# Performance work log

Hardware: AMD Instinct MI355X
Metric: run time of the kernel (lower is better)

Reference implementation:

```python
import jax, jax.numpy as jnp
import numpy as np

DPH, NH = 64, 4           # dim_per_head, num_head -> dim_total = 256
ALPHA_CONV = 0.1          # LeakyReLU alpha in DarknetConv2D_BN_Leaky
ALPHA_DENSE = 0.3         # Keras LeakyReLU default alpha (Dense activation)


def _leaky(x, a):
    return jnp.where(x > 0, x, a * x)


def _cbl(x, W, g, b):
    """1x1 conv (no bias) + inference BatchNorm (folded affine) + LeakyReLU(0.1)."""
    y = jnp.einsum('nwhc,cd->nwhd', x, W)
    return _leaky(y * g + b, ALPHA_CONV)


def setup_inputs() -> dict:
    key = jax.random.key(0)
    ks = jax.random.split(key, 26)
    N, Wg, Hg, C = 16, 64, 64, 256
    D = DPH * NH

    def n(k, shape, s=1.0):
        return jax.random.normal(k, shape, jnp.float32) * s

    return {
        'inputs': n(ks[0], (N, Wg, Hg, C)),
        'style':  n(ks[1], (N, C)),
        'W_dense': n(ks[2], (C, C), 0.05),
        'Wq_c': n(ks[3], (C, D), 0.05), 'gq_c': 1.0 + n(ks[4], (D,), 0.02), 'bq_c': n(ks[5], (D,), 0.02),
        'Wk_c': n(ks[6], (C, D), 0.05), 'gk_c': 1.0 + n(ks[7], (D,), 0.02), 'bk_c': n(ks[8], (D,), 0.02),
        'Wv_c': n(ks[9], (C, D), 0.05), 'gv_c': 1.0 + n(ks[10], (D,), 0.02), 'bv_c': n(ks[11], (D,), 0.02),
        'Wq_p': n(ks[12], (C, D), 0.05), 'gq_p': 1.0 + n(ks[13], (D,), 0.02), 'bq_p': n(ks[14], (D,), 0.02),
        'Wk_p': n(ks[15], (C, D), 0.05), 'gk_p': 1.0 + n(ks[16], (D,), 0.02), 'bk_p': n(ks[17], (D,), 0.02),
        'Wv_p': n(ks[18], (C, D), 0.05), 'gv_p': 1.0 + n(ks[19], (D,), 0.02), 'bv_p': n(ks[20], (D,), 0.02),
        'W_ch':  n(ks[21], (2 * D, D), 0.02),
        'W_pos': n(ks[22], (2 * D, NH), 0.02),
        'W_out': n(ks[23], (2 * D, C), 0.05),
        'g_out': 1.0 + n(ks[24], (C,), 0.02),
        'b_out': n(ks[25], (C,), 0.02),
    }


def reference(inputs, style, W_dense,
              Wq_c, gq_c, bq_c, Wk_c, gk_c, bk_c, Wv_c, gv_c, bv_c,
              Wq_p, gq_p, bq_p, Wk_p, gk_p, bk_p, Wv_p, gv_p, bv_p,
              W_ch, W_pos, W_out, g_out, b_out):
    N, Wg, Hg, C = inputs.shape
    D = DPH * NH
    scale = 1.0 / jnp.sqrt(jnp.float32(DPH))

    # style -> query feature, [N,1,1,C]
    q0 = _leaky(style @ W_dense, ALPHA_DENSE)[:, None, None, :]

    # ---------- channel-wise attention branch ----------
    qc = _cbl(q0, Wq_c, gq_c, bq_c)          # [N,1,1,D]
    kc = _cbl(inputs, Wk_c, gk_c, bk_c)      # [N,W,H,D]
    vc = _cbl(inputs, Wv_c, gv_c, bv_c)      # [N,W,H,D]
    catc = jnp.concatenate([jnp.broadcast_to(qc, kc.shape), kc], axis=-1)  # [N,W,H,2D]
    # einsum('awhd,awhdc->ac') with w broadcast over a,w,h == plain contraction
    a_c = jnp.einsum('nwhd,dc->nc', catc, W_ch) * scale                     # [N,D]
    a_c = jax.nn.softmax(a_c.reshape(N, DPH, NH), axis=1).reshape(N, 1, 1, D)
    o_ch = a_c * vc                                                          # [N,W,H,D]

    # ---------- position-wise attention branch ----------
    qp = _cbl(q0, Wq_p, gq_p, bq_p)
    kp = _cbl(inputs, Wk_p, gk_p, bk_p)
    vp = _cbl(inputs, Wv_p, gv_p, bv_p)
    catp = jnp.concatenate([jnp.broadcast_to(qp, kp.shape), kp], axis=-1)   # [N,W,H,2D]
    a_p = jnp.einsum('nwhd,dm->nwhm', catp, W_pos) * scale                  # [N,W,H,NH]
    a_p = jax.nn.softmax(a_p.reshape(N, Wg * Hg, NH), axis=1)
    a_p = a_p.reshape(N, Wg, Hg, NH, 1)
    o_pos = (a_p * vp.reshape(N, Wg, Hg, NH, DPH)).reshape(N, Wg, Hg, D)

    # ---------- fuse + output 1x1 conv ----------
    out = _cbl(jnp.concatenate([o_ch, o_pos], axis=-1), W_out, g_out, b_out)  # [N,W,H,C]
    return out
```

## Files before the change

### kernel.cpp

```cpp
#include <hip/hip_runtime.h>
#include <hip/hip_bf16.h>

#define PTOT  65536
#define SCALE 0.125f

typedef __attribute__((ext_vector_type(8))) short short8;
typedef __attribute__((ext_vector_type(4))) float f32x4;

__device__ __forceinline__ float leaky(float x, float a) { return x > 0.f ? x : a * x; }

__device__ __forceinline__ unsigned short f2bfbits(float f) {
    __hip_bfloat16 h = __float2bfloat16(f); unsigned short u;
    __builtin_memcpy(&u, &h, 2); return u;
}

__device__ __forceinline__ void gld16(const void* g, void* l) {
    __builtin_amdgcn_global_load_lds(
        (const __attribute__((address_space(1))) unsigned int*)g,
        (__attribute__((address_space(3))) unsigned int*)l, 16, 0, 0);
}

__device__ __forceinline__ void mfma_step64(const char* Aseg, const char* Bs,
                                            int l, int wm, int wn, f32x4 acc[2][4])
{
#pragma unroll
    for (int ks = 0; ks < 2; ++ks) {
        short8 af[2], bfr[4];
        const int c = ks * 4 + (l >> 4);
        const int sw = ((c ^ (l & 7)) << 4);
#pragma unroll
        for (int mf = 0; mf < 2; ++mf)
            af[mf] = *(const short8*)(Aseg + (wm * 32 + mf * 16 + (l & 15)) * 128 + sw);
#pragma unroll
        for (int nf = 0; nf < 4; ++nf)
            bfr[nf] = *(const short8*)(Bs + (wn * 64 + nf * 16 + (l & 15)) * 128 + sw);
#pragma unroll
        for (int mf = 0; mf < 2; ++mf)
#pragma unroll
            for (int nf = 0; nf < 4; ++nf)
                acc[mf][nf] = __builtin_amdgcn_mfma_f32_16x16x32_bf16(af[mf], bfr[nf], acc[mf][nf], 0, 0, 0);
    }
}

__device__ __forceinline__ void stageB(const __hip_bfloat16* Bt, int ldk, int k0,
                                       char* Bs, int w, int l, int cg)
{
#pragma unroll
    for (int pass = 0; pass < 4; ++pass) {
        const int col = w * 8 + (l >> 3) + pass * 64;
        gld16(Bt + (size_t)col * ldk + k0 + cg * 8, Bs + (w * 8 + pass * 64) * 128);
    }
}

__device__ __forceinline__ void stageA64(const __hip_bfloat16* Abf, int pix0, int k0,
                                         char* dst, int w, int l, int cg)
{
    const int row = w * 8 + (l >> 3);
    gld16(Abf + (size_t)(pix0 + row) * 256 + k0 + cg * 8, dst + w * 8 * 128);
}

template<int MODE>
__device__ __forceinline__ void k1_body(int bb, int t,
    const float* __restrict__ vin, const float* __restrict__ W,
    const float* __restrict__ g, const float* __restrict__ bv,
    float* __restrict__ vout, float* s0, float (*pr)[32])
{
    const int n = bb >> 3, c0 = (bb & 7) * 32;
    if (t < 256) s0[t] = vin[n * 256 + t];
    __syncthreads();
    const int kp = t >> 5, ci = t & 31, c = c0 + ci;
    float a = 0.f;
#pragma unroll 8
    for (int i = 0; i < 32; ++i) {
        const int k = kp * 32 + i;
        a += s0[k] * W[k * 256 + c];
    }
    pr[kp][ci] = a;
    __syncthreads();
    if (t < 32) {
        float s = 0.f;
#pragma unroll
        for (int q = 0; q < 8; ++q) s += pr[q][t];
        const int cc = c0 + t;
        if constexpr (MODE == 0)      vout[n * 256 + cc] = leaky(s, 0.3f);
        else if constexpr (MODE == 1) vout[n * 256 + cc] = leaky(s * g[cc] + bv[cc], 0.1f);
        else                          vout[n * 256 + cc] = 4096.f * s;
    }
}

template<int MODE>
__global__ __launch_bounds__(256) void k1g(
    const float* __restrict__ vin, const float* __restrict__ W,
    const float* __restrict__ g, const float* __restrict__ bv,
    float* __restrict__ vout)
{
    __shared__ float s0[256];
    __shared__ float pr[8][32];
    k1_body<MODE>(blockIdx.x, threadIdx.x, vin, W, g, bv, vout, s0, pr);
}

__global__ __launch_bounds__(256) void kW_cvt(
    const float* __restrict__ W0, const float* __restrict__ W1,
    const float* __restrict__ W2, const float* __restrict__ W3,
    const float* __restrict__ Wout,
    __hip_bfloat16* __restrict__ WT4, __hip_bfloat16* __restrict__ WoutT,
    const float* __restrict__ style, const float* __restrict__ W_dense,
    float* __restrict__ s1ws)
{
    __shared__ float s0[256];
    __shared__ float pr[8][32];
    const int b = blockIdx.x, t = threadIdx.x;
    if (b < 1024) {
        const int w = b >> 8, c = b & 255;
        const float* W = (w == 0) ? W0 : (w == 1) ? W1 : (w == 2) ? W2 : W3;
        WT4[((size_t)w * 256 + c) * 256 + t] = __float2bfloat16(W[t * 256 + c]);
    } else if (b < 1280) {
        const int c = b - 1024;
        WoutT[(size_t)c * 512 + t]       = __float2bfloat16(Wout[t * 256 + c]);
        WoutT[(size_t)c * 512 + t + 256] = __float2bfloat16(Wout[(t + 256) * 256 + c]);
    } else {
        k1_body<0>(b - 1280, t, style, W_dense, nullptr, nullptr, s1ws, s0, pr);
    }
}

__global__ __launch_bounds__(512, 4) void kA(
    const float* __restrict__ in, __hip_bfloat16* __restrict__ in_bf,
    const __hip_bfloat16* __restrict__ BkcT, const __hip_bfloat16* __restrict__ BkpT,
    const float* __restrict__ gkc, const float* __restrict__ bkc,
    const float* __restrict__ gkp, const float* __restrict__ bkp,
    const float* __restrict__ W_pos,
    float* __restrict__ partial, float* __restrict__ logits)
{
    __shared__ alignas(16) char smem[73728];
    char* Afull = smem;
    char* Bs    = smem + 32768;
    float* wpos_s = (float*)(smem + 65536);
    float* sc     = (float*)(smem + 69632);

    const int t = threadIdx.x, l = t & 63, w = t >> 6;
    const int pix0 = blockIdx.x * 64;

    for (int e = t; e < 1024; e += 512) wpos_s[e] = W_pos[1024 + e];

    {
        const int row = t >> 3, c = t & 7;
#pragma unroll
        for (int seg = 0; seg < 4; ++seg) {
            const float* p = in + (size_t)(pix0 + row) * 256 + seg * 64 + c * 8;
            const float4 x0 = *(const float4*)p, x1 = *(const float4*)(p + 4);
            short8 v;
            v[0]=(short)f2bfbits(x0.x); v[1]=(short)f2bfbits(x0.y); v[2]=(short)f2bfbits(x0.z); v[3]=(short)f2bfbits(x0.w);
            v[4]=(short)f2bfbits(x1.x); v[5]=(short)f2bfbits(x1.y); v[6]=(short)f2bfbits(x1.z); v[7]=(short)f2bfbits(x1.w);
            *(short8*)(Afull + seg * 8192 + row * 128 + ((c ^ (row & 7)) << 4)) = v;
            *(short8*)(in_bf + (size_t)(pix0 + row) * 256 + seg * 64 + c * 8) = v;
        }
    }

    f32x4 acc[4][4];
#pragma unroll
    for (int i = 0; i < 4; ++i)
#pragma unroll
        for (int j = 0; j < 4; ++j) acc[i][j] = (f32x4)0.f;

    for (int s = 0; s < 8; ++s) {
        __syncthreads();
        {
            const int cg = (l & 3) ^ ((l >> 3) & 3);
#pragma unroll
            for (int p = 0; p < 4; ++p) {
                const int col = w * 16 + (l >> 2) + p * 128;
                const __hip_bfloat16* src = (p < 2)
                    ? BkcT + (size_t)col * 256
                    : BkpT + (size_t)(col - 256) * 256;
                gld16(src + s * 32 + cg * 8, Bs + (size_t)(w * 16 + p * 128) * 64);
            }
        }
        __syncthreads();
        {
            const int c8 = (s & 1) * 4 + (l >> 4);
            const char* Aseg = Afull + (s >> 1) * 8192;
            short8 af[4], bfr[4];
#pragma unroll
            for (int mf = 0; mf < 4; ++mf) {
                const int row = mf * 16 + (l & 15);
                af[mf] = *(const short8*)(Aseg + row * 128 + ((c8 ^ (row & 7)) << 4));
            }
#pragma unroll
            for (int nf = 0; nf < 4; ++nf) {
                const int brow = w * 64 + nf * 16 + (l & 15);
                bfr[nf] = *(const short8*)(Bs + brow * 64 + (((l >> 4) ^ ((brow >> 1) & 3)) << 4));
            }
#pragma unroll
            for (int mf = 0; mf < 4; ++mf)
#pragma unroll
                for (int nf = 0; nf < 4; ++nf)
                    acc[mf][nf] = __builtin_amdgcn_mfma_f32_16x16x32_bf16(af[mf], bfr[nf], acc[mf][nf], 0, 0, 0);
        }
    }

    if (w < 4) {
#pragma unroll
        for (int nf = 0; nf < 4; ++nf) {
            const int col = w * 64 + nf * 16 + (l & 15);
            const float g = gkc[col], bb = bkc[col];
            float cs = 0.f;
#pragma unroll
            for (int mf = 0; mf < 4; ++mf)
#pragma unroll
                for (int r = 0; r < 4; ++r) cs += leaky(acc[mf][nf][r] * g + bb, 0.1f);
            cs += __shfl_xor(cs, 16);
            cs += __shfl_xor(cs, 32);
            if (l < 16) partial[(size_t)blockIdx.x * 256 + col] = cs;
        }
    } else {
#pragma unroll
        for (int mf = 0; mf < 4; ++mf)
#pragma unroll
            for (int r = 0; r < 4; ++r) {
                const int row = mf * 16 + (l >> 4) * 4 + r;
                float pm0 = 0.f, pm1 = 0.f, pm2 = 0.f, pm3 = 0.f;
#pragma unroll
                for (int nf = 0; nf < 4; ++nf) {
                    const int kcol = (w - 4) * 64 + nf * 16 + (l & 15);
                    const float g = gkp[kcol], bb = bkp[kcol];
                    const float v = leaky(acc[mf][nf][r] * g + bb, 0.1f);
                    pm0 += v * wpos_s[kcol * 4 + 0];
                    pm1 += v * wpos_s[kcol * 4 + 1];
                    pm2 += v * wpos_s[kcol * 4 + 2];
                    pm3 += v * wpos_s[kcol * 4 + 3];
                }
#pragma unroll
                for (int mask = 1; mask <= 8; mask <<= 1) {
                    pm0 += __shfl_xor(pm0, mask);
                    pm1 += __shfl_xor(pm1, mask);
                    pm2 += __shfl_xor(pm2, mask);
                    pm3 += __shfl_xor(pm3, mask);
                }
                if ((l & 15) == 0) {
                    float* sp = &sc[row * 16 + (w - 4)];
                    sp[0] = pm0; sp[4] = pm1; sp[8] = pm2; sp[12] = pm3;
                }
            }
    }
    __syncthreads();
    if (t < 256) {
        const int row = t >> 2, m = t & 3;
        const float sum = sc[row * 16 + m * 4 + 0] + sc[row * 16 + m * 4 + 1]
                        + sc[row * 16 + m * 4 + 2] + sc[row * 16 + m * 4 + 3];
        logits[(size_t)(pix0 + row) * 4 + m] = SCALE * sum;
    }
}

__global__ __launch_bounds__(256) void k2bc(
    const float* __restrict__ partial,
    const float* __restrict__ acq, const float* __restrict__ W_ch,
    float* __restrict__ a_c, float* __restrict__ lg)
{
    const int t = threadIdx.x;
    if (blockIdx.x < 16) {
        __shared__ float ks[256], lgs[256];
        const int n = blockIdx.x;
        float s = 0.f;
        for (int tt = 0; tt < 64; ++tt) s += partial[(size_t)(n * 64 + tt) * 256 + t];
        ks[t] = s;
        __syncthreads();
        float bot = 0.f;
        for (int d = 0; d < 256; ++d) bot += ks[d] * W_ch[(256 + d) * 256 + t];
        const float L = SCALE * (acq[n * 256 + t] + bot);
        lgs[t] = L;
        __syncthreads();
        const int nh = t & 3;
        float mx = -1e30f;
        for (int i = 0; i < 64; ++i) mx = fmaxf(mx, lgs[i * 4 + nh]);
        float sum = 0.f;
        for (int i = 0; i < 64; ++i) sum += __expf(lgs[i * 4 + nh] - mx);
        a_c[n * 256 + t] = __expf(L - mx) / sum;
    } else {
        __shared__ float r[256];
        const int bb = blockIdx.x - 16;
        const int n = bb >> 2, m = bb & 3;
        const int base = n * 4096;
        float v[16];
        float mx = -1e30f;
#pragma unroll
        for (int i = 0; i < 16; ++i) {
            v[i] = lg[(size_t)(base + i * 256 + t) * 4 + m];
            mx = fmaxf(mx, v[i]);
        }
        r[t] = mx; __syncthreads();
        for (int s = 128; s > 0; s >>= 1) { if (t < s) r[t] = fmaxf(r[t], r[t + s]); __syncthreads(); }
        mx = r[0]; __syncthreads();
        float sum = 0.f;
#pragma unroll
        for (int i = 0; i < 16; ++i) { v[i] = __expf(v[i] - mx); sum += v[i]; }
        r[t] = sum; __syncthreads();
        for (int s = 128; s > 0; s >>= 1) { if (t < s) r[t] += r[t + s]; __syncthreads(); }
        const float rinv = 1.f / r[0];
#pragma unroll
        for (int i = 0; i < 16; ++i) lg[(size_t)(base + i * 256 + t) * 4 + m] = v[i] * rinv;
    }
}

__global__ __launch_bounds__(512, 4) void kB(
    const __hip_bfloat16* __restrict__ Abf,
    const __hip_bfloat16* __restrict__ BvcT, const __hip_bfloat16* __restrict__ BvpT,
    const __hip_bfloat16* __restrict__ WoutT,
    const float* __restrict__ gvc, const float* __restrict__ bvc,
    const float* __restrict__ gvp, const float* __restrict__ bvp,
    const float* __restrict__ a_c, const float* __restrict__ apos,
    const float* __restrict__ g_out, const float* __restrict__ b_out,
    float* __restrict__ outp)
{
    __shared__ alignas(16) char smem[75776];
    char* As   = smem;
    char* Bs   = smem + 8192;
    char* A2   = smem + 40960;
    float* ac_s = (float*)(smem + 73728);
    float* ap_s = (float*)(smem + 74752);

    const int t = threadIdx.x, l = t & 63, w = t >> 6;
    const int wm = w >> 2, wn = w & 3;
    const int pix0 = blockIdx.x * 64;
    const int n = pix0 >> 12;
    const int cg = (l & 7) ^ ((l >> 3) & 7);

    if (t < 256) {
        ac_s[t] = a_c[n * 256 + t];
        ap_s[t] = apos[(size_t)pix0 * 4 + t];
    }

    f32x4 acc1c[2][4], acc1p[2][4], acc2[2][4];
#pragma unroll
    for (int i = 0; i < 2; ++i)
#pragma unroll
        for (int j = 0; j < 4; ++j) {
            acc1c[i][j] = (f32x4)0.f;
            acc1p[i][j] = (f32x4)0.f;
            acc2[i][j]  = (f32x4)0.f;
        }

    for (int s = 0; s < 4; ++s) {
        __syncthreads();
        stageA64(Abf, pix0, s * 64, As, w, l, cg);
        stageB(BvcT, 256, s * 64, Bs, w, l, cg);
        stageB(BvpT, 256, s * 64, A2, w, l, cg);
        __syncthreads();
        mfma_step64(As, Bs, l, wm, wn, acc1c);
        mfma_step64(As, A2, l, wm, wn, acc1p);
    }
    __syncthreads();

#pragma unroll
    for (int nf = 0; nf < 4; ++nf) {
        const int col = wn * 64 + nf * 16 + (l & 15);
        const float g = gvc[col], bb = bvc[col];
        const int c2 = (col & 63) >> 3, cb = (col & 7) * 2;
        const float sc_c = ac_s[col];
#pragma unroll
        for (int mf = 0; mf < 2; ++mf)
#pragma unroll
            for (int r = 0; r < 4; ++r) {
                const int row = wm * 32 + mf * 16 + (l >> 4) * 4 + r;
                float v = leaky(acc1c[mf][nf][r] * g + bb, 0.1f) * sc_c;
                *(unsigned short*)(A2 + wn * 8192 + row * 128
                                   + ((c2 ^ (row & 7)) << 4) + cb) = f2bfbits(v);
            }
    }
    for (int s = 0; s < 4; ++s) {
        __syncthreads();
        stageB(WoutT, 512, s * 64, Bs, w, l, cg);
        __syncthreads();
        mfma_step64(A2 + s * 8192, Bs, l, wm, wn, acc2);
    }
    __syncthreads();
#pragma unroll
    for (int nf = 0; nf < 4; ++nf) {
        const int col = wn * 64 + nf * 16 + (l & 15);
        const float g = gvp[col], bb = bvp[col];
        const int c2 = (col & 63) >> 3, cb = (col & 7) * 2;
#pragma unroll
        for (int mf = 0; mf < 2; ++mf)
#pragma unroll
            for (int r = 0; r < 4; ++r) {
                const int row = wm * 32 + mf * 16 + (l >> 4) * 4 + r;
                float v = leaky(acc1p[mf][nf][r] * g + bb, 0.1f) * ap_s[row * 4 + wn];
                *(unsigned short*)(A2 + wn * 8192 + row * 128
                                   + ((c2 ^ (row & 7)) << 4) + cb) = f2bfbits(v);
            }
    }
    for (int s = 0; s < 4; ++s) {
        __syncthreads();
        stageB(WoutT, 512, 256 + s * 64, Bs, w, l, cg);
        __syncthreads();
        mfma_step64(A2 + s * 8192, Bs, l, wm, wn, acc2);
    }

#pragma unroll
    for (int nf = 0; nf < 4; ++nf) {
        const int col = wn * 64 + nf * 16 + (l & 15);
        const float g = g_out[col], bb = b_out[col];
#pragma unroll
        for (int mf = 0; mf < 2; ++mf)
#pragma unroll
            for (int r = 0; r < 4; ++r) {
                const int p = pix0 + wm * 32 + mf * 16 + (l >> 4) * 4 + r;
                outp[(size_t)p * 256 + col] = leaky(acc2[mf][nf][r] * g + bb, 0.1f);
            }
    }
}

extern "C" void kernel_launch(void* const* d_in, const int* in_sizes, int n_in,
                              void* d_out, int out_size, void* d_ws, size_t ws_size,
                              hipStream_t stream)
{
    const float* inputs  = (const float*)d_in[0];
    const float* style   = (const float*)d_in[1];
    const float* W_dense = (const float*)d_in[2];
    const float* Wq_c = (const float*)d_in[3];
    const float* gq_c = (const float*)d_in[4];
    const float* bq_c = (const float*)d_in[5];
    const float* Wk_c = (const float*)d_in[6];
    const float* gk_c = (const float*)d_in[7];
    const float* bk_c = (const float*)d_in[8];
    const float* Wv_c = (const float*)d_in[9];
    const float* gv_c = (const float*)d_in[10];
    const float* bv_c = (const float*)d_in[11];
    const float* Wk_p = (const float*)d_in[15];
    const float* gk_p = (const float*)d_in[16];
    const float* bk_p = (const float*)d_in[17];
    const float* Wv_p = (const float*)d_in[18];
    const float* gv_p = (const float*)d_in[19];
    const float* bv_p = (const float*)d_in[20];
    const float* W_ch  = (const float*)d_in[21];
    const float* W_pos = (const float*)d_in[22];
    const float* W_out = (const float*)d_in[23];
    const float* g_out = (const float*)d_in[24];
    const float* b_out = (const float*)d_in[25];

    float* ws = (float*)d_ws;
    float* s1ws    = ws;
    float* qcws    = ws + 4096;
    float* acq     = ws + 8192;
    float* a_c     = ws + 12288;
    float* partial = ws + 16384;
    float* logits  = ws + 278528;
    __hip_bfloat16* in_bf = (__hip_bfloat16*)(ws + 540672);
    __hip_bfloat16* WT4   = (__hip_bfloat16*)(ws + 8929280);
    __hip_bfloat16* WoutT = (__hip_bfloat16*)(ws + 9060352);

    kW_cvt<<<1408, 256, 0, stream>>>(Wk_c, Wv_c, Wk_p, Wv_p, W_out,
                                     WT4, WoutT, style, W_dense, s1ws);
    k1g<1><<<128, 256, 0, stream>>>(s1ws, Wq_c, gq_c, bq_c, qcws);
    k1g<2><<<128, 256, 0, stream>>>(qcws, W_ch, nullptr, nullptr, acq);

    kA<<<1024, 512, 0, stream>>>(inputs, in_bf, WT4, WT4 + 2 * 65536,
                                 gk_c, bk_c, gk_p, bk_p, W_pos, partial, logits);

    k2bc<<<80, 256, 0, stream>>>(partial, acq, W_ch, a_c, logits);

    kB<<<1024, 512, 0, stream>>>(in_bf, WT4 + 65536, WT4 + 3 * 65536, WoutT,
                                 gv_c, bv_c, gv_p, bv_p, a_c, logits,
                                 g_out, b_out, (float*)d_out);
}
```

Measured before the change: 140.2 us.

## Load GEMM B fragments directly from global memory instead of staging through LDS

Both GEMM kernels now read weight (B) fragments straight from global memory into registers and no longer stage them in shared memory, which removes several __syncthreads barriers per k-step. The smaller LDS footprint allows more blocks per CU, and launch bounds are raised from 4 to 6 blocks per CU to match. The cost is more global/L2 traffic, since each wave re-reads weights without sharing them through LDS. Global loads are also less coalesced, and the higher occupancy target may force register spilling.

After: 505.4 us. 260% more time.

```diff
diff --git a/kernel.cpp b/kernel.cpp
--- a/kernel.cpp
+++ b/kernel.cpp
@@ -20,8 +20,9 @@
         (__attribute__((address_space(3))) unsigned int*)l, 16, 0, 0);
 }
 
-__device__ __forceinline__ void mfma_step64(const char* Aseg, const char* Bs,
-                                            int l, int wm, int wn, f32x4 acc[2][4])
+__device__ __forceinline__ void mfma_gB64(const char* Aseg,
+                                          const __hip_bfloat16* __restrict__ Bg, int ldk, int kb,
+                                          int l, int wm, int wn, f32x4 acc[2][4])
 {
 #pragma unroll
     for (int ks = 0; ks < 2; ++ks) {
@@ -32,23 +33,15 @@
         for (int mf = 0; mf < 2; ++mf)
             af[mf] = *(const short8*)(Aseg + (wm * 32 + mf * 16 + (l & 15)) * 128 + sw);
 #pragma unroll
-        for (int nf = 0; nf < 4; ++nf)
-            bfr[nf] = *(const short8*)(Bs + (wn * 64 + nf * 16 + (l & 15)) * 128 + sw);
+        for (int nf = 0; nf < 4; ++nf) {
+            const int col = wn * 64 + nf * 16 + (l & 15);
+            bfr[nf] = *(const short8*)(Bg + (size_t)col * ldk + kb + c * 8);
+        }
 #pragma unroll
         for (int mf = 0; mf < 2; ++mf)
 #pragma unroll
             for (int nf = 0; nf < 4; ++nf)
                 acc[mf][nf] = __builtin_amdgcn_mfma_f32_16x16x32_bf16(af[mf], bfr[nf], acc[mf][nf], 0, 0, 0);
-    }
-}
-
-__device__ __forceinline__ void stageB(const __hip_bfloat16* Bt, int ldk, int k0,
-                                       char* Bs, int w, int l, int cg)
-{
-#pragma unroll
-    for (int pass = 0; pass < 4; ++pass) {
-        const int col = w * 8 + (l >> 3) + pass * 64;
-        gld16(Bt + (size_t)col * ldk + k0 + cg * 8, Bs + (w * 8 + pass * 64) * 128);
     }
 }
 
@@ -123,7 +116,7 @@
     }
 }
 
-__global__ __launch_bounds__(512, 4) void kA(
+__global__ __launch_bounds__(512, 6) void kA(
     const float* __restrict__ in, __hip_bfloat16* __restrict__ in_bf,
     const __hip_bfloat16* __restrict__ BkcT, const __hip_bfloat16* __restrict__ BkpT,
     const float* __restrict__ gkc, const float* __restrict__ bkc,
@@ -131,11 +124,10 @@
     const float* __restrict__ W_pos,
     float* __restrict__ partial, float* __restrict__ logits)
 {
-    __shared__ alignas(16) char smem[73728];
+    __shared__ alignas(16) char smem[40960];
     char* Afull = smem;
-    char* Bs    = smem + 32768;
-    float* wpos_s = (float*)(smem + 65536);
-    float* sc     = (float*)(smem + 69632);
+    float* wpos_s = (float*)(smem + 32768);
+    float* sc     = (float*)(smem + 36864);
 
     const int t = threadIdx.x, l = t & 63, w = t >> 6;
     const int pix0 = blockIdx.x * 64;
@@ -155,6 +147,10 @@
             *(short8*)(in_bf + (size_t)(pix0 + row) * 256 + seg * 64 + c * 8) = v;
         }
     }
+    __syncthreads();
+
+    const __hip_bfloat16* Bw = (w < 4) ? (BkcT + (size_t)(w * 64) * 256)
+                                       : (BkpT + (size_t)((w - 4) * 64) * 256);
 
     f32x4 acc[4][4];
 #pragma unroll
@@ -163,39 +159,22 @@
         for (int j = 0; j < 4; ++j) acc[i][j] = (f32x4)0.f;
 
     for (int s = 0; s < 8; ++s) {
-        __syncthreads();
-        {
-            const int cg = (l & 3) ^ ((l >> 3) & 3);
-#pragma unroll
-            for (int p = 0; p < 4; ++p) {
-                const int col = w * 16 + (l >> 2) + p * 128;
-                const __hip_bfloat16* src = (p < 2)
-                    ? BkcT + (size_t)col * 256
-                    : BkpT + (size_t)(col - 256) * 256;
-                gld16(src + s * 32 + cg * 8, Bs + (size_t)(w * 16 + p * 128) * 64);
-            }
-        }
-        __syncthreads();
-        {
-            const int c8 = (s & 1) * 4 + (l >> 4);
-            const char* Aseg = Afull + (s >> 1) * 8192;
-            short8 af[4], bfr[4];
-#pragma unroll
-            for (int mf = 0; mf < 4; ++mf) {
-                const int row = mf * 16 + (l & 15);
-                af[mf] = *(const short8*)(Aseg + row * 128 + ((c8 ^ (row & 7)) << 4));
-            }
-#pragma unroll
-            for (int nf = 0; nf < 4; ++nf) {
-                const int brow = w * 64 + nf * 16 + (l & 15);
-                bfr[nf] = *(const short8*)(Bs + brow * 64 + (((l >> 4) ^ ((brow >> 1) & 3)) << 4));
-            }
-#pragma unroll
-            for (int mf = 0; mf < 4; ++mf)
-#pragma unroll
-                for (int nf = 0; nf < 4; ++nf)
-                    acc[mf][nf] = __builtin_amdgcn_mfma_f32_16x16x32_bf16(af[mf], bfr[nf], acc[mf][nf], 0, 0, 0);
-        }
+        const int c8 = (s & 1) * 4 + (l >> 4);
+        const char* Aseg = Afull + (s >> 1) * 8192;
+        short8 af[4], bfr[4];
+#pragma unroll
+        for (int mf = 0; mf < 4; ++mf) {
+            const int row = mf * 16 + (l & 15);
+            af[mf] = *(const short8*)(Aseg + row * 128 + ((c8 ^ (row & 7)) << 4));
+        }
+#pragma unroll
+        for (int nf = 0; nf < 4; ++nf)
+            bfr[nf] = *(const short8*)(Bw + (size_t)(nf * 16 + (l & 15)) * 256 + s * 32 + (l >> 4) * 8);
+#pragma unroll
+        for (int mf = 0; mf < 4; ++mf)
+#pragma unroll
+            for (int nf = 0; nf < 4; ++nf)
+                acc[mf][nf] = __builtin_amdgcn_mfma_f32_16x16x32_bf16(af[mf], bfr[nf], acc[mf][nf], 0, 0, 0);
     }
 
     if (w < 4) {
@@ -301,7 +280,7 @@
     }
 }
 
-__global__ __launch_bounds__(512, 4) void kB(
+__global__ __launch_bounds__(512, 6) void kB(
     const __hip_bfloat16* __restrict__ Abf,
     const __hip_bfloat16* __restrict__ BvcT, const __hip_bfloat16* __restrict__ BvpT,
     const __hip_bfloat16* __restrict__ WoutT,
@@ -311,12 +290,11 @@
     const float* __restrict__ g_out, const float* __restrict__ b_out,
     float* __restrict__ outp)
 {
-    __shared__ alignas(16) char smem[75776];
+    __shared__ alignas(16) char smem[43008];
     char* As   = smem;
-    char* Bs   = smem + 8192;
-    char* A2   = smem + 40960;
-    float* ac_s = (float*)(smem + 73728);
-    float* ap_s = (float*)(smem + 74752);
+    char* A2   = smem + 8192;
+    float* ac_s = (float*)(smem + 40960);
+    float* ap_s = (float*)(smem + 41984);
 
     const int t = threadIdx.x, l = t & 63, w = t >> 6;
     const int wm = w >> 2, wn = w & 3;
@@ -342,13 +320,10 @@
     for (int s = 0; s < 4; ++s) {
         __syncthreads();
         stageA64(Abf, pix0, s * 64, As, w, l, cg);
-        stageB(BvcT, 256, s * 64, Bs, w, l, cg);
-        stageB(BvpT, 256, s * 64, A2, w, l, cg);
         __syncthreads();
-        mfma_step64(As, Bs, l, wm, wn, acc1c);
-        mfma_step64(As, A2, l, wm, wn, acc1p);
-    }
-    __syncthreads();
+        mfma_gB64(As, BvcT, 256, s * 64, l, wm, wn, acc1c);
+        mfma_gB64(As, BvpT, 256, s * 64, l, wm, wn, acc1p);
+    }
 
 #pragma unroll
     for (int nf = 0; nf < 4; ++nf) {
@@ -366,12 +341,10 @@
                                    + ((c2 ^ (row & 7)) << 4) + cb) = f2bfbits(v);
             }
     }
-    for (int s = 0; s < 4; ++s) {
-        __syncthreads();
-        stageB(WoutT, 512, s * 64, Bs, w, l, cg);
-        __syncthreads();
-        mfma_step64(A2 + s * 8192, Bs, l, wm, wn, acc2);
-    }
+    __syncthreads();
+#pragma unroll
+    for (int s = 0; s < 4; ++s)
+        mfma_gB64(A2 + s * 8192, WoutT, 512, s * 64, l, wm, wn, acc2);
     __syncthreads();
 #pragma unroll
     for (int nf = 0; nf < 4; ++nf) {
@@ -388,12 +361,10 @@
                                    + ((c2 ^ (row & 7)) << 4) + cb) = f2bfbits(v);
             }
     }
-    for (int s = 0; s < 4; ++s) {
-        __syncthreads();
-        stageB(WoutT, 512, 256 + s * 64, Bs, w, l, cg);
-        __syncthreads();
-        mfma_step64(A2 + s * 8192, Bs, l, wm, wn, acc2);
-    }
+    __syncthreads();
+#pragma unroll
+    for (int s = 0; s < 4; ++s)
+        mfma_gB64(A2 + s * 8192, WoutT, 512, 256 + s * 64, l, wm, wn, acc2);
 
 #pragma unroll
     for (int nf = 0; nf < 4; ++nf) {
```
